# Performance work log

Measured on AMD Instinct MI355X. Metric: run time of the kernel, lower is better.

## Reference

```python
import jax, jax.numpy as jnp
import numpy as np

B, T, D = 4, 2048, 1024
E, K, H = 8, 2, 2048

def setup_inputs() -> dict:
    key = jax.random.key(0)
    ks = jax.random.split(key, 5)
    scale = 0.02
    x = jax.random.normal(ks[0], (B, T, D), dtype=jnp.float32)
    gate_w = jax.random.normal(ks[1], (E, D), dtype=jnp.float32) * scale   # Linear(D->E) weight [out,in]
    w_gate = jax.random.normal(ks[2], (E, H, D), dtype=jnp.float32) * scale
    w_in = jax.random.normal(ks[3], (E, H, D), dtype=jnp.float32) * scale
    w_out = jax.random.normal(ks[4], (E, D, H), dtype=jnp.float32) * scale
    return {"x": x, "gate_w": gate_w, "w_gate": w_gate, "w_in": w_in, "w_out": w_out}

def reference(x, gate_w, w_gate, w_in, w_out):
    # Router: logits (B,T,E) -> top-k -> softmax over the k selected logits
    logits = jnp.einsum('btd,ed->bte', x, gate_w)
    topk_vals, topk_idx = jax.lax.top_k(logits, K)          # (B,T,K)
    routing = jax.nn.softmax(topk_vals, axis=-1)            # (B,T,K)

    out = jnp.zeros_like(x)
    # Masked-matmul: loop over the small fixed expert bank (E=8)
    for e in range(E):
        sel = (topk_idx == e)                               # (B,T,K) bool
        mask = sel.any(axis=-1)                             # (B,T)
        w = jnp.sum(routing * sel.astype(routing.dtype), axis=-1)  # (B,T)
        mx = x * mask[..., None].astype(x.dtype)            # (B,T,D)
        h = jax.nn.silu(jnp.einsum('btd,hd->bth', mx, w_gate[e])) * jnp.einsum('btd,hd->bth', mx, w_in[e])
        out = out + jnp.einsum('bth,dh->btd', h, w_out[e]) * w[..., None]
    return out
```

## Files before the change

kernel.cpp:

```cpp
#include <hip/hip_runtime.h>
#include <stdint.h>
#include <stddef.h>

#define NTOK 8192
#define DDIM 1024
#define NEXP 8
#define HDIM 2048
#define LSTRIDE (NTOK + 256)
#define NCHUNK 128
#define MAXROWS (2 * NTOK + NEXP * 256)

typedef __attribute__((ext_vector_type(4))) float f32x4;
typedef __attribute__((ext_vector_type(8))) short s16x8;
typedef __attribute__((ext_vector_type(4))) short s16x4;

static __device__ __forceinline__ unsigned short f2bf(float f) {
  union { float f; unsigned u; } v; v.f = f;
  unsigned r = v.u + 0x7FFFu + ((v.u >> 16) & 1u);
  return (unsigned short)(r >> 16);
}
static __device__ __forceinline__ float bf2f(unsigned short h) {
  union { unsigned u; float f; } v; v.u = ((unsigned)h) << 16;
  return v.f;
}

static __device__ __forceinline__ void gll16(const void* g, void* l) {
  __builtin_amdgcn_global_load_lds((const __attribute__((address_space(1))) void*)g,
                                   (__attribute__((address_space(3))) void*)l, 16, 0, 0);
}

#define BAR_MID() __builtin_amdgcn_s_barrier()
#define BAR_END() do { __builtin_amdgcn_s_barrier(); __builtin_amdgcn_sched_barrier(0); } while (0)
#define LGKM0() do { asm volatile("s_waitcnt lgkmcnt(0)" ::: "memory"); __builtin_amdgcn_sched_barrier(0); } while (0)
#define VMW6() asm volatile("s_waitcnt vmcnt(6)" ::: "memory")
#define VMW0() asm volatile("s_waitcnt vmcnt(0)" ::: "memory")

__global__ void k_sentinel(float* out) { if (threadIdx.x == 0) out[0] = 1.0e6f; }

__global__ __launch_bounds__(256) void k_prep(const float* __restrict__ x,
    const float* __restrict__ gw,
    const float* __restrict__ wgate, const float* __restrict__ win, const float* __restrict__ wout,
    unsigned short* __restrict__ wgb, unsigned short* __restrict__ wib, unsigned short* __restrict__ wob,
    unsigned* __restrict__ tokE, float2* __restrict__ tokW2, unsigned short* __restrict__ xbf) {
  int b = blockIdx.x;
  if (b >= 2048) {
    const float* srcs[3] = { wgate, win, wout };
    unsigned short* dsts[3] = { wgb, wib, wob };
    int g = (b - 2048) * 256 + threadIdx.x;
    const int stride = 1536 * 256;
#pragma unroll
    for (int it = 0; it < 16; ++it) {
      int arr = g >> 21;
      int idx = g & ((1 << 21) - 1);
      const f32x4* s = (const f32x4*)(srcs[arr] + (size_t)idx * 8);
      f32x4 a = s[0], c = s[1];
      s16x8 o;
      o[0] = f2bf(a[0]); o[1] = f2bf(a[1]); o[2] = f2bf(a[2]); o[3] = f2bf(a[3]);
      o[4] = f2bf(c[0]); o[5] = f2bf(c[1]); o[6] = f2bf(c[2]); o[7] = f2bf(c[3]);
      *(s16x8*)(dsts[arr] + (size_t)idx * 8) = o;
      g += stride;
    }
    return;
  }
  int lane = threadIdx.x & 63;
  int t = b * 4 + (threadIdx.x >> 6);
  const f32x4* x4 = (const f32x4*)x;
  const f32x4* g4 = (const f32x4*)gw;
  f32x4 xr[4];
#pragma unroll
  for (int j = 0; j < 4; ++j) xr[j] = x4[(size_t)t * 256 + j * 64 + lane];
#pragma unroll
  for (int j = 0; j < 4; ++j) {
    s16x4 o;
    o[0] = f2bf(xr[j][0]); o[1] = f2bf(xr[j][1]); o[2] = f2bf(xr[j][2]); o[3] = f2bf(xr[j][3]);
    *(s16x4*)(xbf + (size_t)t * DDIM + (j * 64 + lane) * 4) = o;
  }
  float le[8];
#pragma unroll
  for (int e = 0; e < 8; ++e) {
    float p = 0.f;
#pragma unroll
    for (int j = 0; j < 4; ++j) {
      f32x4 g = g4[e * 256 + j * 64 + lane];
      p += xr[j][0] * g[0] + xr[j][1] * g[1] + xr[j][2] * g[2] + xr[j][3] * g[3];
    }
#pragma unroll
    for (int off = 32; off > 0; off >>= 1) p += __shfl_xor(p, off, 64);
    le[e] = p;
  }
  if (lane == 0) {
    int i0 = 0; float v0 = le[0];
#pragma unroll
    for (int e = 1; e < 8; ++e) if (le[e] > v0) { v0 = le[e]; i0 = e; }
    int i1 = -1; float v1 = 0.f;
#pragma unroll
    for (int e = 0; e < 8; ++e) if (e != i0 && (i1 < 0 || le[e] > v1)) { v1 = le[e]; i1 = e; }
    float bb = __expf(v1 - v0);
    float s = 1.f + bb;
    tokE[t] = (unsigned)i0 | ((unsigned)i1 << 8);
    tokW2[t] = make_float2(1.f / s, bb / s);
  }
}

__global__ __launch_bounds__(64) void k_hist(const unsigned* __restrict__ tokE,
                                             int* __restrict__ cntTable) {
  __shared__ int c8[NEXP];
  int tid = threadIdx.x, c = blockIdx.x;
  if (tid < NEXP) c8[tid] = 0;
  __syncthreads();
  unsigned v = tokE[c * 64 + tid];
  atomicAdd(&c8[v & 255], 1);
  atomicAdd(&c8[(v >> 8) & 255], 1);
  __syncthreads();
  if (tid < NEXP) cntTable[tid * NCHUNK + c] = c8[tid];
}

__global__ __launch_bounds__(64) void k_scan(const int* __restrict__ cntTable,
                                             int* __restrict__ ctrl, int* __restrict__ cbL) {
  __shared__ int tot[NEXP];
  int e = threadIdx.x;
  if (e < NEXP) {
    int s = 0;
    for (int c = 0; c < NCHUNK; ++c) s += cntTable[e * NCHUNK + c];
    tot[e] = s; ctrl[e] = s;
  }
  __syncthreads();
  if (e == 0) {
    int acc = 0;
    for (int q = 0; q < NEXP; ++q) { ctrl[8 + q] = acc; acc += (tot[q] + 255) & ~255; }
  }
  if (e < NEXP) {
    int run = 0;
    for (int c = 0; c < NCHUNK; ++c) { cbL[e * NCHUNK + c] = run; run += cntTable[e * NCHUNK + c]; }
  }
}

__global__ __launch_bounds__(64) void k_scatter(const unsigned* __restrict__ tokE,
    const float2* __restrict__ tokW2, const int* __restrict__ cbL,
    int* __restrict__ listTok, float* __restrict__ listW, int* __restrict__ listSlot) {
  __shared__ int lcnt[NEXP];
  int tid = threadIdx.x, c = blockIdx.x;
  if (tid < NEXP) lcnt[tid] = 0;
  __syncthreads();
  int t = c * 64 + tid;
  unsigned v = tokE[t];
  int e0 = v & 255, e1 = (v >> 8) & 255;
  float2 w = tokW2[t];
  int l0 = atomicAdd(&lcnt[e0], 1);
  int l1 = atomicAdd(&lcnt[e1], 1);
  int i0 = cbL[e0 * NCHUNK + c] + l0;
  int i1 = cbL[e1 * NCHUNK + c] + l1;
  listTok[e0 * LSTRIDE + i0] = t; listW[e0 * LSTRIDE + i0] = w.x; listSlot[e0 * LSTRIDE + i0] = 0;
  listTok[e1 * LSTRIDE + i1] = t; listW[e1 * LSTRIDE + i1] = w.y; listSlot[e1 * LSTRIDE + i1] = 1;
}

__global__ __launch_bounds__(512, 2) void k_gemm1(const unsigned short* __restrict__ xbf,
    const unsigned short* __restrict__ wg, const unsigned short* __restrict__ wi,
    const int* __restrict__ ctrl, const int* __restrict__ listTok,
    unsigned short* __restrict__ hbuf) {
  int bid = blockIdx.x;
  int xc = bid & 7, w = bid >> 3;
  int nb = w & 15;
  int p = ((w >> 4) << 3) | xc;
  int m = p & 31, e = p >> 5;
  int cnt = ctrl[e];
  int m0 = m << 8;
  if (m0 >= cnt) return;
  int rowb = ctrl[8 + e];
  int n0 = nb << 7;

  __shared__ __align__(16) char lds[131072];
  char* ldsc = &lds[0];

  int tid = threadIdx.x, lane = tid & 63, wv = tid >> 6;
  int wm = wv >> 1, wn = wv & 1;

  int srow = tid >> 3;
  int scol = (((tid & 7) ^ ((tid >> 3) & 7)) << 4);
  int sdst = wv << 10;
  const char* pA[2][2];
  const char* pBg[2];
  const char* pBi[2];
#pragma unroll
  for (int rg = 0; rg < 2; ++rg)
#pragma unroll
    for (int sb = 0; sb < 2; ++sb) {
      int tok = listTok[e * LSTRIDE + m0 + rg * 128 + sb * 64 + srow];
      pA[rg][sb] = (const char*)xbf + (size_t)tok * 2048 + scol;
    }
#pragma unroll
  for (int sb = 0; sb < 2; ++sb) {
    pBg[sb] = (const char*)wg + ((size_t)e * HDIM + n0 + sb * 64 + srow) * 2048 + scol;
    pBi[sb] = (const char*)wi + ((size_t)e * HDIM + n0 + sb * 64 + srow) * 2048 + scol;
  }

  int rowB = (lane & 15) << 7;
  int mk = (lane & 7) << 4;
  int q16 = (lane >> 4) << 4;
  int c0 = q16 ^ mk, c1 = (q16 + 64) ^ mk;
  int aO0 = 32768 + (wm >> 1) * 16384 + ((wm & 1) * 64) * 128 + rowB + c0;
  int aO1 = aO0 - c0 + c1;
  int gO0 = (wn * 64) * 128 + rowB + c0;
  int gO1 = gO0 - c0 + c1;
  int iO0 = 16384 + (wn * 64) * 128 + rowB + c0;
  int iO1 = iO0 - c0 + c1;

#define G1_STA(BUF, RG, KO) do { \
    gll16(pA[RG][0] + (KO), ldsc + (BUF) + 32768 + (RG) * 16384 + sdst); \
    gll16(pA[RG][1] + (KO), ldsc + (BUF) + 32768 + (RG) * 16384 + 8192 + sdst); } while (0)
#define G1_STG(BUF, KO) do { \
    gll16(pBg[0] + (KO), ldsc + (BUF) + sdst); \
    gll16(pBg[1] + (KO), ldsc + (BUF) + 8192 + sdst); } while (0)
#define G1_STI(BUF, KO) do { \
    gll16(pBi[0] + (KO), ldsc + (BUF) + 16384 + sdst); \
    gll16(pBi[1] + (KO), ldsc + (BUF) + 16384 + 8192 + sdst); } while (0)
#define G1_RDA(BUF) { _Pragma("unroll") for (int mf = 0; mf < 4; ++mf) { \
    af[mf][0] = *(const s16x8*)(ldsc + (BUF) + aO0 + mf * 2048); \
    af[mf][1] = *(const s16x8*)(ldsc + (BUF) + aO1 + mf * 2048); } }
#define G1_RDG(BUF) { _Pragma("unroll") for (int nf = 0; nf < 4; ++nf) { \
    bg[nf][0] = *(const s16x8*)(ldsc + (BUF) + gO0 + nf * 2048); \
    bg[nf][1] = *(const s16x8*)(ldsc + (BUF) + gO1 + nf * 2048); } }
#define G1_RDI(BUF) { _Pragma("unroll") for (int nf = 0; nf < 4; ++nf) { \
    bi[nf][0] = *(const s16x8*)(ldsc + (BUF) + iO0 + nf * 2048); \
    bi[nf][1] = *(const s16x8*)(ldsc + (BUF) + iO1 + nf * 2048); } }
#define G1_MMG(NH) do { __builtin_amdgcn_s_setprio(1); \
    _Pragma("unroll") for (int mf = 0; mf < 4; ++mf) _Pragma("unroll") for (int nf = 0; nf < 2; ++nf) { \
      accg[mf][(NH)*2+nf] = __builtin_amdgcn_mfma_f32_16x16x32_bf16(af[mf][0], bg[(NH)*2+nf][0], accg[mf][(NH)*2+nf], 0, 0, 0); \
      accg[mf][(NH)*2+nf] = __builtin_amdgcn_mfma_f32_16x16x32_bf16(af[mf][1], bg[(NH)*2+nf][1], accg[mf][(NH)*2+nf], 0, 0, 0); } \
    __builtin_amdgcn_s_setprio(0); } while (0)
#define G1_MMI(NH) do { __builtin_amdgcn_s_setprio(1); \
    _Pragma("unroll") for (int mf = 0; mf < 4; ++mf) _Pragma("unroll") for (int nf = 0; nf < 2; ++nf) { \
      acci[mf][(NH)*2+nf] = __builtin_amdgcn_mfma_f32_16x16x32_bf16(af[mf][0], bi[(NH)*2+nf][0], acci[mf][(NH)*2+nf], 0, 0, 0); \
      acci[mf][(NH)*2+nf] = __builtin_amdgcn_mfma_f32_16x16x32_bf16(af[mf][1], bi[(NH)*2+nf][1], acci[mf][(NH)*2+nf], 0, 0, 0); } \
    __builtin_amdgcn_s_setprio(0); } while (0)

  f32x4 accg[4][4], acci[4][4];
#pragma unroll
  for (int a = 0; a < 4; ++a)
#pragma unroll
    for (int b = 0; b < 4; ++b) { accg[a][b] = (f32x4){0.f,0.f,0.f,0.f}; acci[a][b] = (f32x4){0.f,0.f,0.f,0.f}; }
  s16x8 af[4][2], bg[4][2], bi[4][2];

  G1_STG(0, 0); G1_STA(0, 0, 0); G1_STI(0, 0); G1_STA(0, 1, 0);
  G1_STG(65536, 128); G1_STA(65536, 0, 128); G1_STI(65536, 128);
  VMW6();
  BAR_END();

  const int NIT = DDIM / 128;
  for (int i = 0; i < NIT; ++i) {
    const int koC = (2 * i + 1) * 128, koA = (2 * i + 2) * 128, koB = (2 * i + 3) * 128;
    const bool more = (i + 1 < NIT);
    G1_RDA(0); G1_RDG(0);
    G1_STA(65536, 1, koC);
    BAR_MID(); LGKM0();
    G1_MMG(0);
    BAR_END();
    if (more) G1_STG(0, koA);
    BAR_MID();
    G1_MMG(1);
    BAR_END();
    G1_RDI(0);
    if (more) G1_STA(0, 0, koA);
    BAR_MID(); LGKM0();
    G1_MMI(0);
    BAR_END();
    if (more) G1_STI(0, koA);
    BAR_MID();
    G1_MMI(1);
    if (more) VMW6(); else VMW0();
    BAR_END();
    G1_RDA(65536); G1_RDG(65536);
    if (more) G1_STA(0, 1, koA);
    BAR_MID(); LGKM0();
    G1_MMG(0);
    BAR_END();
    if (more) G1_STG(65536, koB);
    BAR_MID();
    G1_MMG(1);
    BAR_END();
    G1_RDI(65536);
    if (more) G1_STA(65536, 0, koB);
    BAR_MID(); LGKM0();
    G1_MMI(0);
    BAR_END();
    if (more) G1_STI(65536, koB);
    BAR_MID();
    G1_MMI(1);
    if (more) VMW6();
    BAR_END();
  }

#pragma unroll
  for (int mf = 0; mf < 4; ++mf)
#pragma unroll
    for (int j = 0; j < 4; ++j) {
      int r = wm * 64 + mf * 16 + ((lane >> 4) << 2) + j;
      size_t rowoff = (size_t)(rowb + m0 + r) * HDIM;
#pragma unroll
      for (int nf = 0; nf < 4; ++nf) {
        int cc = n0 + wn * 64 + nf * 16 + (lane & 15);
        float g = accg[mf][nf][j];
        float iv = acci[mf][nf][j];
        float hv = g / (1.f + __expf(-g)) * iv;
        hbuf[rowoff + cc] = f2bf(hv);
      }
    }
#undef G1_STA
#undef G1_STG
#undef G1_STI
#undef G1_RDA
#undef G1_RDG
#undef G1_RDI
#undef G1_MMG
#undef G1_MMI
}

__global__ __launch_bounds__(512, 2) void k_gemm2(const unsigned short* __restrict__ hbuf,
    const unsigned short* __restrict__ wo, const int* __restrict__ ctrl,
    const int* __restrict__ listTok, const float* __restrict__ listW,
    const int* __restrict__ listSlot, unsigned short* __restrict__ ybuf) {
  int bid = blockIdx.x;
  int xc = bid & 7, w = bid >> 3;
  int nb = w & 3;
  int p = ((w >> 2) << 3) | xc;
  int m = p & 31, e = p >> 5;
  int cnt = ctrl[e];
  int m0 = m << 8;
  if (m0 >= cnt) return;
  int rowb = ctrl[8 + e];
  int n0 = nb << 8;

  __shared__ __align__(16) char lds[131072];
  char* ldsc = &lds[0];

  int tid = threadIdx.x, lane = tid & 63, wv = tid >> 6;
  int wm = wv >> 2, wn = wv & 3;

  int srow = tid >> 3;
  int scol = (((tid & 7) ^ ((tid >> 3) & 7)) << 4);
  int sdst = wv << 10;
  const char* pA[2][2];
  const char* pB[2][2];
#pragma unroll
  for (int rg = 0; rg < 2; ++rg)
#pragma unroll
    for (int sb = 0; sb < 2; ++sb) {
      int tr = rg * 128 + sb * 64 + srow;
      pA[rg][sb] = (const char*)hbuf + (size_t)(rowb + m0 + tr) * 4096 + scol;
      pB[rg][sb] = (const char*)wo + ((size_t)e * DDIM + n0 + tr) * 4096 + scol;
    }

  int rowB = (lane & 15) << 7;
  int mk = (lane & 7) << 4;
  int q16 = (lane >> 4) << 4;
  int c0 = q16 ^ mk, c1 = (q16 + 64) ^ mk;
  int aO0 = 32768 + wm * 16384 + rowB + c0;
  int aO1 = aO0 - c0 + c1;
  int bO0 = (wn >> 1) * 16384 + ((wn & 1) * 64) * 128 + rowB + c0;
  int bO1 = bO0 - c0 + c1;

#define G2_STA(BUF, RG, KO) do { \
    gll16(pA[RG][0] + (KO), ldsc + (BUF) + 32768 + (RG) * 16384 + sdst); \
    gll16(pA[RG][1] + (KO), ldsc + (BUF) + 32768 + (RG) * 16384 + 8192 + sdst); } while (0)
#define G2_STB(BUF, RG, KO) do { \
    gll16(pB[RG][0] + (KO), ldsc + (BUF) + (RG) * 16384 + sdst); \
    gll16(pB[RG][1] + (KO), ldsc + (BUF) + (RG) * 16384 + 8192 + sdst); } while (0)
#define G2_RDA(BUF, MH) { _Pragma("unroll") for (int mf = 0; mf < 4; ++mf) { \
    af[mf][0] = *(const s16x8*)(ldsc + (BUF) + aO0 + ((MH) * 64 + mf * 16) * 128); \
    af[mf][1] = *(const s16x8*)(ldsc + (BUF) + aO1 + ((MH) * 64 + mf * 16) * 128); } }
#define G2_RDB(BUF) { _Pragma("unroll") for (int nf = 0; nf < 4; ++nf) { \
    bf[nf][0] = *(const s16x8*)(ldsc + (BUF) + bO0 + nf * 2048); \
    bf[nf][1] = *(const s16x8*)(ldsc + (BUF) + bO1 + nf * 2048); } }
#define G2_MM(MH, NH) do { __builtin_amdgcn_s_setprio(1); \
    _Pragma("unroll") for (int mf = 0; mf < 4; ++mf) _Pragma("unroll") for (int nf = 0; nf < 2; ++nf) { \
      acc[(MH)*4+mf][(NH)*2+nf] = __builtin_amdgcn_mfma_f32_16x16x32_bf16(af[mf][0], bf[(NH)*2+nf][0], acc[(MH)*4+mf][(NH)*2+nf], 0, 0, 0); \
      acc[(MH)*4+mf][(NH)*2+nf] = __builtin_amdgcn_mfma_f32_16x16x32_bf16(af[mf][1], bf[(NH)*2+nf][1], acc[(MH)*4+mf][(NH)*2+nf], 0, 0, 0); } \
    __builtin_amdgcn_s_setprio(0); } while (0)

  f32x4 acc[8][4];
#pragma unroll
  for (int a = 0; a < 8; ++a)
#pragma unroll
    for (int b = 0; b < 4; ++b) acc[a][b] = (f32x4){0.f,0.f,0.f,0.f};
  s16x8 af[4][2], bf[4][2];

  G2_STB(0, 0, 0); G2_STB(0, 1, 0); G2_STA(0, 0, 0); G2_STA(0, 1, 0);
  G2_STB(65536, 0, 128); G2_STB(65536, 1, 128); G2_STA(65536, 0, 128);
  VMW6();
  BAR_END();

  const int NIT = HDIM / 128;
  for (int i = 0; i < NIT; ++i) {
    const int koC = (2 * i + 1) * 128, koA = (2 * i + 2) * 128, koB = (2 * i + 3) * 128;
    const bool more = (i + 1 < NIT);
    G2_RDA(0, 0); G2_RDB(0);
    G2_STA(65536, 1, koC);
    BAR_MID(); LGKM0();
    G2_MM(0, 0);
    BAR_END();
    if (more) G2_STB(0, 0, koA);
    BAR_MID();
    G2_MM(0, 1);
    BAR_END();
    G2_RDA(0, 1);
    if (more) G2_STB(0, 1, koA);
    BAR_MID(); LGKM0();
    G2_MM(1, 0);
    BAR_END();
    if (more) G2_STA(0, 0, koA);
    BAR_MID();
    G2_MM(1, 1);
    if (more) VMW6(); else VMW0();
    BAR_END();
    G2_RDA(65536, 0); G2_RDB(65536);
    if (more) G2_STA(0, 1, koA);
    BAR_MID(); LGKM0();
    G2_MM(0, 0);
    BAR_END();
    if (more) G2_STB(65536, 0, koB);
    BAR_MID();
    G2_MM(0, 1);
    BAR_END();
    G2_RDA(65536, 1);
    if (more) G2_STB(65536, 1, koB);
    BAR_MID(); LGKM0();
    G2_MM(1, 0);
    BAR_END();
    if (more) G2_STA(65536, 0, koB);
    BAR_MID();
    G2_MM(1, 1);
    if (more) VMW6();
    BAR_END();
  }

#pragma unroll
  for (int mf = 0; mf < 8; ++mf)
#pragma unroll
    for (int j = 0; j < 4; ++j) {
      int r = wm * 128 + mf * 16 + ((lane >> 4) << 2) + j;
      int mrow = m0 + r;
      if (mrow < cnt) {
        int tok = listTok[e * LSTRIDE + mrow];
        float wgt = listW[e * LSTRIDE + mrow];
        int slot = listSlot[e * LSTRIDE + mrow];
        size_t base = ((size_t)slot * NTOK + tok) * DDIM + n0 + wn * 64;
#pragma unroll
        for (int nf = 0; nf < 4; ++nf)
          ybuf[base + nf * 16 + (lane & 15)] = f2bf(acc[mf][nf][j] * wgt);
      }
    }
#undef G2_STA
#undef G2_STB
#undef G2_RDA
#undef G2_RDB
#undef G2_MM
}

__global__ __launch_bounds__(256) void k_reduce(const unsigned short* __restrict__ ybuf,
                                                float* __restrict__ out, int n8) {
  int i = blockIdx.x * blockDim.x + threadIdx.x;
  int stride = gridDim.x * blockDim.x;
  const unsigned short* y0 = ybuf;
  const unsigned short* y1 = ybuf + (size_t)NTOK * DDIM;
  for (; i < n8; i += stride) {
    s16x8 a = *(const s16x8*)(y0 + (size_t)i * 8);
    s16x8 b = *(const s16x8*)(y1 + (size_t)i * 8);
    f32x4 o0, o1;
#pragma unroll
    for (int j = 0; j < 4; ++j) o0[j] = bf2f((unsigned short)a[j]) + bf2f((unsigned short)b[j]);
#pragma unroll
    for (int j = 0; j < 4; ++j) o1[j] = bf2f((unsigned short)a[4 + j]) + bf2f((unsigned short)b[4 + j]);
    f32x4* d = (f32x4*)(out + (size_t)i * 8);
    d[0] = o0; d[1] = o1;
  }
}

extern "C" void kernel_launch(void* const* d_in, const int* in_sizes, int n_in,
                              void* d_out, int out_size, void* d_ws, size_t ws_size,
                              hipStream_t stream) {
  const float* x     = (const float*)d_in[0];
  const float* gw    = (const float*)d_in[1];
  const float* wgate = (const float*)d_in[2];
  const float* win   = (const float*)d_in[3];
  const float* wout  = (const float*)d_in[4];
  float* out = (float*)d_out;

  const size_t LBYTES     = (size_t)NEXP * LSTRIDE * 4;
  const size_t OFF_LIST   = 256;
  const size_t OFF_LISTW  = OFF_LIST + LBYTES;
  const size_t ZERO_BYTES = OFF_LISTW;
  const size_t OFF_SLOT   = OFF_LISTW + LBYTES;
  const size_t OFF_CB     = OFF_SLOT + LBYTES;
  const size_t OFF_CT     = OFF_CB + 4096;
  const size_t OFF_TE     = OFF_CT + 4096;
  const size_t OFF_TW     = OFF_TE + (size_t)NTOK * 4;
  const size_t OFF_XBF = (size_t)1 << 20;
  const size_t OFF_WG  = OFF_XBF + (size_t)NTOK * DDIM * 2;
  const size_t OFF_WI  = OFF_WG + (size_t)NEXP * HDIM * DDIM * 2;
  const size_t OFF_WO  = OFF_WI + (size_t)NEXP * HDIM * DDIM * 2;
  const size_t OFF_H   = OFF_WO + (size_t)NEXP * DDIM * HDIM * 2;
  const size_t OFF_Y   = OFF_WG;
  const size_t TOTAL   = OFF_H + (size_t)MAXROWS * HDIM * 2;

  if (ws_size < TOTAL) { k_sentinel<<<1, 64, 0, stream>>>(out); return; }

  char* ws = (char*)d_ws;
  int* ctrl            = (int*)ws;
  int* listTok         = (int*)(ws + OFF_LIST);
  float* listW         = (float*)(ws + OFF_LISTW);
  int* listSlot        = (int*)(ws + OFF_SLOT);
  int* cbL             = (int*)(ws + OFF_CB);
  int* cntTable        = (int*)(ws + OFF_CT);
  unsigned* tokE       = (unsigned*)(ws + OFF_TE);
  float2* tokW2        = (float2*)(ws + OFF_TW);
  unsigned short* xbf  = (unsigned short*)(ws + OFF_XBF);
  unsigned short* wgb  = (unsigned short*)(ws + OFF_WG);
  unsigned short* wib  = (unsigned short*)(ws + OFF_WI);
  unsigned short* wob  = (unsigned short*)(ws + OFF_WO);
  unsigned short* hbuf = (unsigned short*)(ws + OFF_H);
  unsigned short* ybuf = (unsigned short*)(ws + OFF_Y);

  hipMemsetAsync(ws, 0, ZERO_BYTES, stream);

  k_prep<<<3584, 256, 0, stream>>>(x, gw, wgate, win, wout, wgb, wib, wob, tokE, tokW2, xbf);
  k_hist<<<NCHUNK, 64, 0, stream>>>(tokE, cntTable);
  k_scan<<<1, 64, 0, stream>>>(cntTable, ctrl, cbL);
  k_scatter<<<NCHUNK, 64, 0, stream>>>(tokE, tokW2, cbL, listTok, listW, listSlot);

  k_gemm1<<<16 * 32 * NEXP, 512, 0, stream>>>(xbf, wgb, wib, ctrl, listTok, hbuf);
  k_gemm2<<<4 * 32 * NEXP, 512, 0, stream>>>(hbuf, wob, ctrl, listTok, listW, listSlot, ybuf);
  k_reduce<<<512, 256, 0, stream>>>(ybuf, out, NTOK * DDIM / 8);
}
```

Measured before the change: 405.7 us.

## Shrink gemm2 tile to 256x128 and switch GEMMs to 3D grid indexing

The down-projection GEMM moves from a 256x256 output tile to a 256x128 tile. That cuts accumulators in half, shrinks LDS from 128 KB to 96 KB, and simplifies the double-buffered pipeline to one full-stage load per half iteration. Both GEMMs drop the swizzled 1D block ordering, which grouped blocks for L2 locality, in favour of a plain dim3(n, m, expert) grid. The intent is more blocks and better occupancy and tail balance for gemm2, at the cost of re-reading the A operand (hbuf) twice as often and losing the cache-friendly block ordering.

```diff
diff --git a/kernel.cpp b/kernel.cpp
--- a/kernel.cpp
+++ b/kernel.cpp
@@ -158,16 +158,12 @@
     const unsigned short* __restrict__ wg, const unsigned short* __restrict__ wi,
     const int* __restrict__ ctrl, const int* __restrict__ listTok,
     unsigned short* __restrict__ hbuf) {
-  int bid = blockIdx.x;
-  int xc = bid & 7, w = bid >> 3;
-  int nb = w & 15;
-  int p = ((w >> 4) << 3) | xc;
-  int m = p & 31, e = p >> 5;
+  int e = blockIdx.z;
   int cnt = ctrl[e];
-  int m0 = m << 8;
+  int m0 = blockIdx.y * 256;
   if (m0 >= cnt) return;
   int rowb = ctrl[8 + e];
-  int n0 = nb << 7;
+  int n0 = blockIdx.x * 128;
 
   __shared__ __align__(16) char lds[131072];
   char* ldsc = &lds[0];
@@ -319,125 +315,102 @@
     const unsigned short* __restrict__ wo, const int* __restrict__ ctrl,
     const int* __restrict__ listTok, const float* __restrict__ listW,
     const int* __restrict__ listSlot, unsigned short* __restrict__ ybuf) {
-  int bid = blockIdx.x;
-  int xc = bid & 7, w = bid >> 3;
-  int nb = w & 3;
-  int p = ((w >> 2) << 3) | xc;
-  int m = p & 31, e = p >> 5;
+  int e = blockIdx.z;
   int cnt = ctrl[e];
-  int m0 = m << 8;
+  int m0 = blockIdx.y * 256;
   if (m0 >= cnt) return;
   int rowb = ctrl[8 + e];
-  int n0 = nb << 8;
-
-  __shared__ __align__(16) char lds[131072];
+  int n0 = blockIdx.x * 128;
+
+  __shared__ __align__(16) char lds[98304];
   char* ldsc = &lds[0];
+#define BUF2 49152
 
   int tid = threadIdx.x, lane = tid & 63, wv = tid >> 6;
-  int wm = wv >> 2, wn = wv & 3;
+  int wm = wv >> 1, wn = wv & 1;
 
   int srow = tid >> 3;
   int scol = (((tid & 7) ^ ((tid >> 3) & 7)) << 4);
   int sdst = wv << 10;
   const char* pA[2][2];
-  const char* pB[2][2];
+  const char* pB[2];
 #pragma unroll
   for (int rg = 0; rg < 2; ++rg)
 #pragma unroll
-    for (int sb = 0; sb < 2; ++sb) {
-      int tr = rg * 128 + sb * 64 + srow;
-      pA[rg][sb] = (const char*)hbuf + (size_t)(rowb + m0 + tr) * 4096 + scol;
-      pB[rg][sb] = (const char*)wo + ((size_t)e * DDIM + n0 + tr) * 4096 + scol;
-    }
+    for (int sb = 0; sb < 2; ++sb)
+      pA[rg][sb] = (const char*)hbuf + (size_t)(rowb + m0 + rg * 128 + sb * 64 + srow) * 4096 + scol;
+#pragma unroll
+  for (int sb = 0; sb < 2; ++sb)
+    pB[sb] = (const char*)wo + ((size_t)e * DDIM + n0 + sb * 64 + srow) * 4096 + scol;
 
   int rowB = (lane & 15) << 7;
   int mk = (lane & 7) << 4;
   int q16 = (lane >> 4) << 4;
   int c0 = q16 ^ mk, c1 = (q16 + 64) ^ mk;
-  int aO0 = 32768 + wm * 16384 + rowB + c0;
+  int aO0 = wm * 8192 + rowB + c0;
   int aO1 = aO0 - c0 + c1;
-  int bO0 = (wn >> 1) * 16384 + ((wn & 1) * 64) * 128 + rowB + c0;
+  int bO0 = 32768 + wn * 8192 + rowB + c0;
   int bO1 = bO0 - c0 + c1;
 
 #define G2_STA(BUF, RG, KO) do { \
-    gll16(pA[RG][0] + (KO), ldsc + (BUF) + 32768 + (RG) * 16384 + sdst); \
-    gll16(pA[RG][1] + (KO), ldsc + (BUF) + 32768 + (RG) * 16384 + 8192 + sdst); } while (0)
-#define G2_STB(BUF, RG, KO) do { \
-    gll16(pB[RG][0] + (KO), ldsc + (BUF) + (RG) * 16384 + sdst); \
-    gll16(pB[RG][1] + (KO), ldsc + (BUF) + (RG) * 16384 + 8192 + sdst); } while (0)
-#define G2_RDA(BUF, MH) { _Pragma("unroll") for (int mf = 0; mf < 4; ++mf) { \
-    af[mf][0] = *(const s16x8*)(ldsc + (BUF) + aO0 + ((MH) * 64 + mf * 16) * 128); \
-    af[mf][1] = *(const s16x8*)(ldsc + (BUF) + aO1 + ((MH) * 64 + mf * 16) * 128); } }
+    gll16(pA[RG][0] + (KO), ldsc + (BUF) + (RG) * 16384 + sdst); \
+    gll16(pA[RG][1] + (KO), ldsc + (BUF) + (RG) * 16384 + 8192 + sdst); } while (0)
+#define G2_STB(BUF, KO) do { \
+    gll16(pB[0] + (KO), ldsc + (BUF) + 32768 + sdst); \
+    gll16(pB[1] + (KO), ldsc + (BUF) + 32768 + 8192 + sdst); } while (0)
+#define G2_RDA(BUF) { _Pragma("unroll") for (int mf = 0; mf < 4; ++mf) { \
+    af[mf][0] = *(const s16x8*)(ldsc + (BUF) + aO0 + mf * 2048); \
+    af[mf][1] = *(const s16x8*)(ldsc + (BUF) + aO1 + mf * 2048); } }
 #define G2_RDB(BUF) { _Pragma("unroll") for (int nf = 0; nf < 4; ++nf) { \
     bf[nf][0] = *(const s16x8*)(ldsc + (BUF) + bO0 + nf * 2048); \
     bf[nf][1] = *(const s16x8*)(ldsc + (BUF) + bO1 + nf * 2048); } }
-#define G2_MM(MH, NH) do { __builtin_amdgcn_s_setprio(1); \
+#define G2_MM(NH) do { __builtin_amdgcn_s_setprio(1); \
     _Pragma("unroll") for (int mf = 0; mf < 4; ++mf) _Pragma("unroll") for (int nf = 0; nf < 2; ++nf) { \
-      acc[(MH)*4+mf][(NH)*2+nf] = __builtin_amdgcn_mfma_f32_16x16x32_bf16(af[mf][0], bf[(NH)*2+nf][0], acc[(MH)*4+mf][(NH)*2+nf], 0, 0, 0); \
-      acc[(MH)*4+mf][(NH)*2+nf] = __builtin_amdgcn_mfma_f32_16x16x32_bf16(af[mf][1], bf[(NH)*2+nf][1], acc[(MH)*4+mf][(NH)*2+nf], 0, 0, 0); } \
+      acc[mf][(NH)*2+nf] = __builtin_amdgcn_mfma_f32_16x16x32_bf16(af[mf][0], bf[(NH)*2+nf][0], acc[mf][(NH)*2+nf], 0, 0, 0); \
+      acc[mf][(NH)*2+nf] = __builtin_amdgcn_mfma_f32_16x16x32_bf16(af[mf][1], bf[(NH)*2+nf][1], acc[mf][(NH)*2+nf], 0, 0, 0); } \
     __builtin_amdgcn_s_setprio(0); } while (0)
 
-  f32x4 acc[8][4];
-#pragma unroll
-  for (int a = 0; a < 8; ++a)
+  f32x4 acc[4][4];
+#pragma unroll
+  for (int a = 0; a < 4; ++a)
 #pragma unroll
     for (int b = 0; b < 4; ++b) acc[a][b] = (f32x4){0.f,0.f,0.f,0.f};
   s16x8 af[4][2], bf[4][2];
 
-  G2_STB(0, 0, 0); G2_STB(0, 1, 0); G2_STA(0, 0, 0); G2_STA(0, 1, 0);
-  G2_STB(65536, 0, 128); G2_STB(65536, 1, 128); G2_STA(65536, 0, 128);
+  G2_STA(0, 0, 0); G2_STA(0, 1, 0); G2_STB(0, 0);
+  G2_STA(BUF2, 0, 128); G2_STA(BUF2, 1, 128); G2_STB(BUF2, 128);
   VMW6();
   BAR_END();
 
   const int NIT = HDIM / 128;
   for (int i = 0; i < NIT; ++i) {
-    const int koC = (2 * i + 1) * 128, koA = (2 * i + 2) * 128, koB = (2 * i + 3) * 128;
+    const int koA = (2 * i + 2) * 128, koB = (2 * i + 3) * 128;
     const bool more = (i + 1 < NIT);
-    G2_RDA(0, 0); G2_RDB(0);
-    G2_STA(65536, 1, koC);
+    G2_RDA(0); G2_RDB(0);
     BAR_MID(); LGKM0();
-    G2_MM(0, 0);
-    BAR_END();
-    if (more) G2_STB(0, 0, koA);
+    G2_MM(0);
+    BAR_END();
+    if (more) { G2_STA(0, 0, koA); G2_STA(0, 1, koA); G2_STB(0, koA); }
     BAR_MID();
-    G2_MM(0, 1);
-    BAR_END();
-    G2_RDA(0, 1);
-    if (more) G2_STB(0, 1, koA);
+    G2_MM(1);
+    if (more) VMW6(); else VMW0();
+    BAR_END();
+    G2_RDA(BUF2); G2_RDB(BUF2);
     BAR_MID(); LGKM0();
-    G2_MM(1, 0);
-    BAR_END();
-    if (more) G2_STA(0, 0, koA);
+    G2_MM(0);
+    BAR_END();
+    if (more) { G2_STA(BUF2, 0, koB); G2_STA(BUF2, 1, koB); G2_STB(BUF2, koB); }
     BAR_MID();
-    G2_MM(1, 1);
-    if (more) VMW6(); else VMW0();
-    BAR_END();
-    G2_RDA(65536, 0); G2_RDB(65536);
-    if (more) G2_STA(0, 1, koA);
-    BAR_MID(); LGKM0();
-    G2_MM(0, 0);
-    BAR_END();
-    if (more) G2_STB(65536, 0, koB);
-    BAR_MID();
-    G2_MM(0, 1);
-    BAR_END();
-    G2_RDA(65536, 1);
-    if (more) G2_STB(65536, 1, koB);
-    BAR_MID(); LGKM0();
-    G2_MM(1, 0);
-    BAR_END();
-    if (more) G2_STA(65536, 0, koB);
-    BAR_MID();
-    G2_MM(1, 1);
-    if (more) VMW6();
-    BAR_END();
-  }
-
-#pragma unroll
-  for (int mf = 0; mf < 8; ++mf)
+    G2_MM(1);
+    VMW6();
+    BAR_END();
+  }
+
+#pragma unroll
+  for (int mf = 0; mf < 4; ++mf)
 #pragma unroll
     for (int j = 0; j < 4; ++j) {
-      int r = wm * 128 + mf * 16 + ((lane >> 4) << 2) + j;
+      int r = wm * 64 + mf * 16 + ((lane >> 4) << 2) + j;
       int mrow = m0 + r;
       if (mrow < cnt) {
         int tok = listTok[e * LSTRIDE + mrow];
@@ -454,6 +427,7 @@
 #undef G2_RDA
 #undef G2_RDB
 #undef G2_MM
+#undef BUF2
 }
 
 __global__ __launch_bounds__(256) void k_reduce(const unsigned short* __restrict__ ybuf,
@@ -527,7 +501,7 @@
   k_scan<<<1, 64, 0, stream>>>(cntTable, ctrl, cbL);
   k_scatter<<<NCHUNK, 64, 0, stream>>>(tokE, tokW2, cbL, listTok, listW, listSlot);
 
-  k_gemm1<<<16 * 32 * NEXP, 512, 0, stream>>>(xbf, wgb, wib, ctrl, listTok, hbuf);
-  k_gemm2<<<4 * 32 * NEXP, 512, 0, stream>>>(hbuf, wob, ctrl, listTok, listW, listSlot, ybuf);
+  k_gemm1<<<dim3(HDIM / 128, NTOK / 256, NEXP), 512, 0, stream>>>(xbf, wgb, wib, ctrl, listTok, hbuf);
+  k_gemm2<<<dim3(DDIM / 128, NTOK / 256, NEXP), 512, 0, stream>>>(hbuf, wob, ctrl, listTok, listW, listSlot, ybuf);
   k_reduce<<<512, 256, 0, stream>>>(ybuf, out, NTOK * DDIM / 8);
 }
```

Measured after the change: 365.7 us. 9.9% less time.
